# Kernel optimization log

Hardware: AMD Instinct MI355X
Metric: run time of the kernel (lower is better)

Reference implementation:

```python
import jax, jax.numpy as jnp
import numpy as np


def _resize_bilinear(x, h, w):
    # matches F.upsample(mode='bilinear', align_corners=False) (half-pixel centers)
    return jax.image.resize(x, (x.shape[0], x.shape[1], h, w), method='bilinear')


def _build_volume_2d(fl, fr, maxdisp):
    # fl, fr: [B,C,H,W] -> cost [B,D,H,W], D=maxdisp (stride=1)
    B, C, H, W = fl.shape
    d = jnp.arange(maxdisp)
    src = jnp.arange(W)[None, :] - d[:, None]          # [D,W]
    valid = (src >= 0).astype(fl.dtype)
    src_c = jnp.clip(src, 0, W - 1)
    fr_sh = fr[:, :, :, src_c] * valid                  # [B,C,H,D,W]; zeros where w<d
    cost = jnp.abs(fl[:, :, :, None, :] - fr_sh).sum(axis=1)  # [B,H,D,W]
    return jnp.transpose(cost, (0, 2, 1, 3))            # [B,D,H,W]


def _warp(fr, disp):
    # fr: [B,C,H,W]; disp: [B,K,H,W] horizontal disparity (sample at x - disp)
    # bilinear along W, zero padding (grid_sample semantics, align_corners=True grid)
    B, C, H, W = fr.shape
    xs = jnp.arange(W, dtype=fr.dtype)[None, None, None, :] - disp   # [B,K,H,W]
    x0 = jnp.floor(xs)
    w1 = xs - x0                                        # frac weight for right neighbor
    x0i = x0.astype(jnp.int32)
    x1i = x0i + 1
    v0 = ((x0i >= 0) & (x0i < W)).astype(fr.dtype)
    v1 = ((x1i >= 0) & (x1i < W)).astype(fr.dtype)
    x0c = jnp.clip(x0i, 0, W - 1)
    x1c = jnp.clip(x1i, 0, W - 1)

    def gather(idx):  # idx [B,K,H,W] -> [B,K,C,H,W]
        idxb = jnp.broadcast_to(idx[:, :, None, :, :], (B, idx.shape[1], C, H, W))
        return jnp.take_along_axis(fr[:, None], idxb, axis=-1)

    g0 = gather(x0c) * v0[:, :, None]
    g1 = gather(x1c) * v1[:, :, None]
    return g0 * (1.0 - w1)[:, :, None] + g1 * w1[:, :, None]   # [B,K,C,H,W]


def _build_volume_2d3(fl, fr, maxdisp, disp):
    # fl, fr: [B,C,H,W]; disp: [B,1,H,W] coarse disparity. K = 2*maxdisp-1 shifts.
    shifts = jnp.arange(-maxdisp + 1, maxdisp, dtype=fl.dtype)       # [K]
    bd = disp - shifts[None, :, None, None]                          # [B,K,H,W]
    warped = _warp(fr, bd)                                           # [B,K,C,H,W]
    return jnp.abs(fl[:, None] - warped).sum(axis=2)                 # [B,K,H,W]


def _regress(cost, start, end):
    # softmax(-cost) over disparity axis, weighted sum with disp values [start,end)
    p = jax.nn.softmax(-cost, axis=1)
    dvals = jnp.arange(start, end, dtype=cost.dtype)[None, :, None, None]
    return jnp.sum(p * dvals, axis=1, keepdims=True)                 # [B,1,H,W]


def setup_inputs() -> dict:
    key = jax.random.key(0)
    k = jax.random.split(key, 4)
    return {
        "feat_l0": jax.random.normal(k[0], (4, 32, 64, 128), dtype=jnp.float32),
        "feat_r0": jax.random.normal(k[1], (4, 32, 64, 128), dtype=jnp.float32),
        "feat_l1": jax.random.normal(k[2], (4, 32, 128, 256), dtype=jnp.float32),
        "feat_r1": jax.random.normal(k[3], (4, 32, 128, 256), dtype=jnp.float32),
        "img_h": 512,
        "img_w": 1024,
        "maxdisp0": 12,
        "maxdisp1": 3,
    }


def reference(feat_l0, feat_r0, feat_l1, feat_r1, img_h, img_w, maxdisp0, maxdisp1):
    H0 = feat_l0.shape[2]
    H1, W1 = feat_l1.shape[2], feat_l1.shape[3]

    cost0 = _build_volume_2d(feat_l0, feat_r0, maxdisp0)             # [B,D0,H0,W0]
    pred_low0 = _regress(cost0, 0, maxdisp0) * (img_h / H0)
    pred0 = _resize_bilinear(pred_low0, img_h, img_w)                # [B,1,img_h,img_w]

    # ---- scale 1: residual cost volume via warp around coarse disparity ----
    wflow = _resize_bilinear(pred0, H1, W1) * (H1 / img_h)           # [B,1,H1,W1]
    cost1 = _build_volume_2d3(feat_l1, feat_r1, maxdisp1, wflow)     # [B,2*D1-1,H1,W1]
    pred_low1 = _regress(cost1, -maxdisp1 + 1, maxdisp1) * (img_h / H1)
    pred1 = _resize_bilinear(pred_low1, img_h, img_w) + pred0

    return (pred0, pred1)
```

## Files before the change

### kernel.cpp

```cpp
#include <hip/hip_runtime.h>

#define NB 4
#define NC 32
#define H0 64
#define W0 128
#define D0 12
#define H1 128
#define W1 256
#define NK 5
#define IMH 512
#define IMW 1024

#define FR0_STRIDE 84
#define FR0_GUARD  16
#define FR1_STRIDE 288
#define FR1_GUARD  28

typedef __attribute__((address_space(3))) uint32_t as3_u32;
typedef const __attribute__((address_space(1))) uint32_t as1_u32;

__device__ __forceinline__ float bilin(const float* __restrict__ img, int H, int W,
                                       float sy, float sx) {
    float y0f = floorf(sy), x0f = floorf(sx);
    float fy = sy - y0f, fx = sx - x0f;
    int y0 = (int)y0f, x0 = (int)x0f;
    int y0c = min(max(y0, 0), H - 1);
    int y1c = min(max(y0 + 1, 0), H - 1);
    int x0c = min(max(x0, 0), W - 1);
    int x1c = min(max(x0 + 1, 0), W - 1);
    float v00 = img[y0c * W + x0c];
    float v01 = img[y0c * W + x1c];
    float v10 = img[y1c * W + x0c];
    float v11 = img[y1c * W + x1c];
    float a = v00 * (1.f - fx) + v01 * fx;
    float b = v10 * (1.f - fx) + v11 * fx;
    return a * (1.f - fy) + b * fy;
}

__global__ __launch_bounds__(512) void k_cost0(const float* __restrict__ fl,
                                               const float* __restrict__ fr,
                                               float* __restrict__ pl0) {
    const int blk = blockIdx.x;
    const int row = blk >> 1;
    const int half = blk & 1;
    const int w0 = half * 64;
    const int b = row >> 6, h = row & (H0 - 1);
    const int tid = threadIdx.x;
    __shared__ float frs[NC][FR0_STRIDE];

    const size_t rowbase = ((size_t)b * NC * H0 + h) * W0;

#pragma unroll
    for (int i = 0; i < 2; ++i) {
        int idx = i * 512 + tid;
        if (idx < NC * 20) {
            int c = idx / 20, q = idx - c * 20;
            int colg = w0 - 16 + q * 4;
            float4 v = make_float4(0.f, 0.f, 0.f, 0.f);
            if (colg >= 0)
                v = *(const float4*)(fr + rowbase + (size_t)c * (H0 * W0) + colg);
            *(float4*)&frs[c][q * 4] = v;
        }
    }
    __syncthreads();

    const int wloc = tid >> 3, g = tid & 7;
    float cost[D0];
#pragma unroll
    for (int d = 0; d < D0; ++d) cost[d] = 0.f;
#pragma unroll
    for (int j = 0; j < 4; ++j) {
        int c = g + 8 * j;
        float flv = fl[rowbase + (size_t)c * (H0 * W0) + w0 + wloc];
        const float* sr = &frs[c][FR0_GUARD + wloc];
#pragma unroll
        for (int d = 0; d < D0; ++d)
            cost[d] += fabsf(flv - sr[-d]);
    }
#pragma unroll
    for (int d = 0; d < D0; ++d) {
        cost[d] += __shfl_xor(cost[d], 1);
        cost[d] += __shfl_xor(cost[d], 2);
        cost[d] += __shfl_xor(cost[d], 4);
    }
    if (g == 0) {
        float m = cost[0];
#pragma unroll
        for (int d = 1; d < D0; ++d) m = fminf(m, cost[d]);
        float s = 0.f, sd = 0.f;
#pragma unroll
        for (int d = 0; d < D0; ++d) {
            float e = expf(m - cost[d]);
            s += e;
            sd += (float)d * e;
        }
        pl0[(size_t)row * W0 + w0 + wloc] = 8.f * (sd / s);
    }
}

__global__ __launch_bounds__(512) void k_cost1(const float* __restrict__ fl,
                                               const float* __restrict__ fr,
                                               const float* __restrict__ pl0,
                                               float* __restrict__ pl1) {
    const int blk = blockIdx.x;
    const int b = blk >> 7, oy = blk & (H1 - 1);
    const int tid = threadIdx.x;
    __shared__ float frs1p[NC][FR1_STRIDE];
    __shared__ float ytmp[W0];
    __shared__ float wfl[W1];

    const size_t rowbase1 = ((size_t)b * NC * H1 + oy) * W1;

    {
        const int wave = tid >> 6, lane = tid & 63;
#pragma unroll
        for (int j = 0; j < 4; ++j) {
            int c = wave * 4 + j;
            const float* src = fr + rowbase1 + (size_t)c * (H1 * W1) + lane * 4;
            as3_u32* dst = (as3_u32*)(&frs1p[c][FR1_GUARD]);
            __builtin_amdgcn_global_load_lds((as1_u32*)src, dst, 16, 0, 0);
        }
    }

#pragma unroll
    for (int i = 0; i < 2; ++i) {
        int idx = i * 512 + tid;
        int r = idx >> 5, q = idx & 31;
        int col = (q < FR1_GUARD) ? q : (FR1_GUARD + W1 + (q - FR1_GUARD));
        frs1p[r][col] = 0.f;
    }

    if (tid < W0) {
        const float* p0b = pl0 + (size_t)b * H0 * W0;
        int m = oy >> 1;
        int r0, r1, r2;
        float wy0, wy1, wy2;
        if (oy == 0) {
            r0 = 0; r1 = 0; r2 = 1;
            wy0 = 0.f; wy1 = 27.625f / 28.f; wy2 = 0.375f / 28.f;
        } else if (oy == H1 - 1) {
            r0 = H0 - 2; r1 = H0 - 1; r2 = H0 - 1;
            wy0 = 0.375f / 28.f; wy1 = 27.625f / 28.f; wy2 = 0.f;
        } else {
            r0 = max(m - 1, 0); r1 = m; r2 = min(m + 1, H0 - 1);
            if (oy & 1) { wy0 = 0.375f / 32.f; wy1 = 23.25f / 32.f; wy2 = 8.375f / 32.f; }
            else        { wy0 = 8.375f / 32.f; wy1 = 23.25f / 32.f; wy2 = 0.375f / 32.f; }
        }
        ytmp[tid] = wy0 * p0b[r0 * W0 + tid] + wy1 * p0b[r1 * W0 + tid]
                  + wy2 * p0b[r2 * W0 + tid];
    }
    __syncthreads();

    if (tid < W1) {
        int ox = tid, n = ox >> 1;
        int c0, c1, c2;
        float wx0, wx1, wx2;
        if (ox == 0) {
            c0 = 0; c1 = 0; c2 = 1;
            wx0 = 0.f; wx1 = 27.625f / 28.f; wx2 = 0.375f / 28.f;
        } else if (ox == W1 - 1) {
            c0 = W0 - 2; c1 = W0 - 1; c2 = W0 - 1;
            wx0 = 0.375f / 28.f; wx1 = 27.625f / 28.f; wx2 = 0.f;
        } else {
            c0 = max(n - 1, 0); c1 = n; c2 = min(n + 1, W0 - 1);
            if (ox & 1) { wx0 = 0.375f / 32.f; wx1 = 23.25f / 32.f; wx2 = 8.375f / 32.f; }
            else        { wx0 = 8.375f / 32.f; wx1 = 23.25f / 32.f; wx2 = 0.375f / 32.f; }
        }
        wfl[ox] = 0.25f * (wx0 * ytmp[c0] + wx1 * ytmp[c1] + wx2 * ytmp[c2]);
    }
    __syncthreads();

    {
        const int w = tid >> 1, h = tid & 1;
        float disp = wfl[w];
        float xs = (float)w - disp;
        float xbf = floorf(xs);
        float f = xs - xbf;
        int xb = (int)xbf;
        const float* sr = &frs1p[0][FR1_GUARD + xb - 2];

        float cost[NK];
#pragma unroll
        for (int k = 0; k < NK; ++k) cost[k] = 0.f;
#pragma unroll
        for (int j = 0; j < 16; ++j) {
            int c = 2 * j + h;
            float flv = fl[rowbase1 + (size_t)c * (H1 * W1) + w];
            const float* row = sr + c * FR1_STRIDE;
            float g0 = row[0], g1 = row[1], g2 = row[2];
            float g3 = row[3], g4 = row[4], g5 = row[5];
            cost[0] += fabsf(flv - (g0 + f * (g1 - g0)));
            cost[1] += fabsf(flv - (g1 + f * (g2 - g1)));
            cost[2] += fabsf(flv - (g2 + f * (g3 - g2)));
            cost[3] += fabsf(flv - (g3 + f * (g4 - g3)));
            cost[4] += fabsf(flv - (g4 + f * (g5 - g4)));
        }
#pragma unroll
        for (int k = 0; k < NK; ++k) cost[k] += __shfl_xor(cost[k], 1);
        if (h == 0) {
            float m = cost[0];
#pragma unroll
            for (int k = 1; k < NK; ++k) m = fminf(m, cost[k]);
            float s = 0.f, sd = 0.f;
#pragma unroll
            for (int k = 0; k < NK; ++k) {
                float e = expf(m - cost[k]);
                s += e;
                sd += (float)(k - 2) * e;
            }
            pl1[(size_t)blk * W1 + w] = 4.f * (sd / s);
        }
    }
}

__global__ void k_final(const float* __restrict__ pl0, const float* __restrict__ pl1,
                        float* __restrict__ out) {
    const int NPX = NB * IMH * IMW;
    int t = blockIdx.x * blockDim.x + threadIdx.x;
    if (t >= NPX / 4) return;
    int xq = t & (IMW / 4 - 1);
    int tmp = t >> 8;
    int y = tmp & (IMH - 1);
    int b = tmp >> 9;

    const float* p0b = pl0 + (size_t)b * H0 * W0;
    const float* p1b = pl1 + (size_t)b * H1 * W1;
    float sy0 = (y + 0.5f) * 0.125f - 0.5f;
    float sy1 = (y + 0.5f) * 0.25f - 0.5f;

    float v0[4], v1[4];
#pragma unroll
    for (int i = 0; i < 4; ++i) {
        int x = xq * 4 + i;
        float sx0 = (x + 0.5f) * 0.125f - 0.5f;
        float sx1 = (x + 0.5f) * 0.25f - 0.5f;
        float p0 = bilin(p0b, H0, W0, sy0, sx0);
        v0[i] = p0;
        v1[i] = bilin(p1b, H1, W1, sy1, sx1) + p0;
    }
    ((float4*)out)[t] = make_float4(v0[0], v0[1], v0[2], v0[3]);
    ((float4*)(out + NPX))[t] = make_float4(v1[0], v1[1], v1[2], v1[3]);
}

extern "C" void kernel_launch(void* const* d_in, const int* in_sizes, int n_in,
                              void* d_out, int out_size, void* d_ws, size_t ws_size,
                              hipStream_t stream) {
    const float* fl0 = (const float*)d_in[0];
    const float* fr0 = (const float*)d_in[1];
    const float* fl1 = (const float*)d_in[2];
    const float* fr1 = (const float*)d_in[3];
    float* out = (float*)d_out;

    float* ws = (float*)d_ws;
    float* pl0 = ws;
    float* pl1 = ws + 32768;

    k_cost0<<<NB * H0 * 2, 512, 0, stream>>>(fl0, fr0, pl0);
    k_cost1<<<NB * H1, 512, 0, stream>>>(fl1, fr1, pl0, pl1);

    int n4 = NB * IMH * IMW / 4;
    k_final<<<(n4 + 255) / 256, 256, 0, stream>>>(pl0, pl1, out);
}
```

Baseline: 26.62 us.

## Separable row-interpolated upsampling in final kernel and hoist fl loads before LDS staging

The final upsample kernel now maps one block to one output row. It first interpolates the two source rows vertically into shared memory, then each thread does only a horizontal lerp from LDS, which replaces four global gathers per pixel per scale. The cost kernels issue their left-feature global loads early, before the shared-memory staging and barrier, so that load latency overlaps the staging. This holds more registers (16 floats in cost1), which may lower occupancy.

```diff
diff --git a/kernel.cpp b/kernel.cpp
--- a/kernel.cpp
+++ b/kernel.cpp
@@ -19,24 +19,6 @@
 typedef __attribute__((address_space(3))) uint32_t as3_u32;
 typedef const __attribute__((address_space(1))) uint32_t as1_u32;
 
-__device__ __forceinline__ float bilin(const float* __restrict__ img, int H, int W,
-                                       float sy, float sx) {
-    float y0f = floorf(sy), x0f = floorf(sx);
-    float fy = sy - y0f, fx = sx - x0f;
-    int y0 = (int)y0f, x0 = (int)x0f;
-    int y0c = min(max(y0, 0), H - 1);
-    int y1c = min(max(y0 + 1, 0), H - 1);
-    int x0c = min(max(x0, 0), W - 1);
-    int x1c = min(max(x0 + 1, 0), W - 1);
-    float v00 = img[y0c * W + x0c];
-    float v01 = img[y0c * W + x1c];
-    float v10 = img[y1c * W + x0c];
-    float v11 = img[y1c * W + x1c];
-    float a = v00 * (1.f - fx) + v01 * fx;
-    float b = v10 * (1.f - fx) + v11 * fx;
-    return a * (1.f - fy) + b * fy;
-}
-
 __global__ __launch_bounds__(512) void k_cost0(const float* __restrict__ fl,
                                                const float* __restrict__ fr,
                                                float* __restrict__ pl0) {
@@ -50,6 +32,13 @@
 
     const size_t rowbase = ((size_t)b * NC * H0 + h) * W0;
 
+    const int wloc = tid >> 3, g = tid & 7;
+
+    float flv[4];
+#pragma unroll
+    for (int j = 0; j < 4; ++j)
+        flv[j] = fl[rowbase + (size_t)(g + 8 * j) * (H0 * W0) + w0 + wloc];
+
 #pragma unroll
     for (int i = 0; i < 2; ++i) {
         int idx = i * 512 + tid;
@@ -64,18 +53,16 @@
     }
     __syncthreads();
 
-    const int wloc = tid >> 3, g = tid & 7;
     float cost[D0];
 #pragma unroll
     for (int d = 0; d < D0; ++d) cost[d] = 0.f;
 #pragma unroll
     for (int j = 0; j < 4; ++j) {
         int c = g + 8 * j;
-        float flv = fl[rowbase + (size_t)c * (H0 * W0) + w0 + wloc];
         const float* sr = &frs[c][FR0_GUARD + wloc];
 #pragma unroll
         for (int d = 0; d < D0; ++d)
-            cost[d] += fabsf(flv - sr[-d]);
+            cost[d] += fabsf(flv[j] - sr[-d]);
     }
 #pragma unroll
     for (int d = 0; d < D0; ++d) {
@@ -121,6 +108,12 @@
             __builtin_amdgcn_global_load_lds((as1_u32*)src, dst, 16, 0, 0);
         }
     }
+
+    const int w = tid >> 1, hh = tid & 1;
+    float flv[16];
+#pragma unroll
+    for (int j = 0; j < 16; ++j)
+        flv[j] = fl[rowbase1 + (size_t)(2 * j + hh) * (H1 * W1) + w];
 
 #pragma unroll
     for (int i = 0; i < 2; ++i) {
@@ -171,7 +164,6 @@
     __syncthreads();
 
     {
-        const int w = tid >> 1, h = tid & 1;
         float disp = wfl[w];
         float xs = (float)w - disp;
         float xbf = floorf(xs);
@@ -184,20 +176,20 @@
         for (int k = 0; k < NK; ++k) cost[k] = 0.f;
 #pragma unroll
         for (int j = 0; j < 16; ++j) {
-            int c = 2 * j + h;
-            float flv = fl[rowbase1 + (size_t)c * (H1 * W1) + w];
+            int c = 2 * j + hh;
             const float* row = sr + c * FR1_STRIDE;
             float g0 = row[0], g1 = row[1], g2 = row[2];
             float g3 = row[3], g4 = row[4], g5 = row[5];
-            cost[0] += fabsf(flv - (g0 + f * (g1 - g0)));
-            cost[1] += fabsf(flv - (g1 + f * (g2 - g1)));
-            cost[2] += fabsf(flv - (g2 + f * (g3 - g2)));
-            cost[3] += fabsf(flv - (g3 + f * (g4 - g3)));
-            cost[4] += fabsf(flv - (g4 + f * (g5 - g4)));
+            float flvj = flv[j];
+            cost[0] += fabsf(flvj - (g0 + f * (g1 - g0)));
+            cost[1] += fabsf(flvj - (g1 + f * (g2 - g1)));
+            cost[2] += fabsf(flvj - (g2 + f * (g3 - g2)));
+            cost[3] += fabsf(flvj - (g3 + f * (g4 - g3)));
+            cost[4] += fabsf(flvj - (g5 * f + g4 * (1.f - f)));
         }
 #pragma unroll
         for (int k = 0; k < NK; ++k) cost[k] += __shfl_xor(cost[k], 1);
-        if (h == 0) {
+        if (hh == 0) {
             float m = cost[0];
 #pragma unroll
             for (int k = 1; k < NK; ++k) m = fminf(m, cost[k]);
@@ -213,33 +205,65 @@
     }
 }
 
-__global__ void k_final(const float* __restrict__ pl0, const float* __restrict__ pl1,
-                        float* __restrict__ out) {
-    const int NPX = NB * IMH * IMW;
-    int t = blockIdx.x * blockDim.x + threadIdx.x;
-    if (t >= NPX / 4) return;
-    int xq = t & (IMW / 4 - 1);
-    int tmp = t >> 8;
-    int y = tmp & (IMH - 1);
-    int b = tmp >> 9;
+__global__ __launch_bounds__(256) void k_final(const float* __restrict__ pl0,
+                                               const float* __restrict__ pl1,
+                                               float* __restrict__ out) {
+    const int blk = blockIdx.x;
+    const int b = blk >> 9, y = blk & (IMH - 1);
+    const int tid = threadIdx.x;
+    __shared__ float a0[W0];
+    __shared__ float a1[W1];
 
     const float* p0b = pl0 + (size_t)b * H0 * W0;
     const float* p1b = pl1 + (size_t)b * H1 * W1;
+
     float sy0 = (y + 0.5f) * 0.125f - 0.5f;
+    float y0f = floorf(sy0);
+    float fy0 = sy0 - y0f;
+    int r0 = (int)y0f;
+    int r0c = min(max(r0, 0), H0 - 1), r1c = min(max(r0 + 1, 0), H0 - 1);
+
     float sy1 = (y + 0.5f) * 0.25f - 0.5f;
+    float y1f = floorf(sy1);
+    float fy1 = sy1 - y1f;
+    int s0 = (int)y1f;
+    int s0c = min(max(s0, 0), H1 - 1), s1c = min(max(s0 + 1, 0), H1 - 1);
+
+    if (tid < W0) {
+        float u = p0b[r0c * W0 + tid], v = p0b[r1c * W0 + tid];
+        a0[tid] = u + fy0 * (v - u);
+    }
+    {
+        float u = p1b[s0c * W1 + tid], v = p1b[s1c * W1 + tid];
+        a1[tid] = u + fy1 * (v - u);
+    }
+    __syncthreads();
 
     float v0[4], v1[4];
 #pragma unroll
     for (int i = 0; i < 4; ++i) {
-        int x = xq * 4 + i;
+        int x = tid * 4 + i;
         float sx0 = (x + 0.5f) * 0.125f - 0.5f;
+        float x0f = floorf(sx0);
+        float fx0 = sx0 - x0f;
+        int c0 = (int)x0f;
+        int c0c = min(max(c0, 0), W0 - 1), c1c = min(max(c0 + 1, 0), W0 - 1);
+        float p0 = a0[c0c] + fx0 * (a0[c1c] - a0[c0c]);
+
         float sx1 = (x + 0.5f) * 0.25f - 0.5f;
-        float p0 = bilin(p0b, H0, W0, sy0, sx0);
+        float x1f = floorf(sx1);
+        float fx1 = sx1 - x1f;
+        int d0 = (int)x1f;
+        int d0c = min(max(d0, 0), W1 - 1), d1c = min(max(d0 + 1, 0), W1 - 1);
+        float p1 = a1[d0c] + fx1 * (a1[d1c] - a1[d0c]);
+
         v0[i] = p0;
-        v1[i] = bilin(p1b, H1, W1, sy1, sx1) + p0;
-    }
+        v1[i] = p1 + p0;
+    }
+    const size_t NPXQ = (size_t)NB * IMH * IMW / 4;
+    size_t t = (size_t)blk * 256 + tid;
     ((float4*)out)[t] = make_float4(v0[0], v0[1], v0[2], v0[3]);
-    ((float4*)(out + NPX))[t] = make_float4(v1[0], v1[1], v1[2], v1[3]);
+    ((float4*)out)[NPXQ + t] = make_float4(v1[0], v1[1], v1[2], v1[3]);
 }
 
 extern "C" void kernel_launch(void* const* d_in, const int* in_sizes, int n_in,
@@ -257,7 +281,5 @@
 
     k_cost0<<<NB * H0 * 2, 512, 0, stream>>>(fl0, fr0, pl0);
     k_cost1<<<NB * H1, 512, 0, stream>>>(fl1, fr1, pl0, pl1);
-
-    int n4 = NB * IMH * IMW / 4;
-    k_final<<<(n4 + 255) / 256, 256, 0, stream>>>(pl0, pl1, out);
-}
+    k_final<<<NB * IMH, 256, 0, stream>>>(pl0, pl1, out);
+}
```

After: 26.27 us. Within noise of the previous version (-1.3%).
